# Performance work log

Measured on AMD Instinct MI355X. Metric: run time of the kernel, lower is better.

## Reference

```python
import jax, jax.numpy as jnp
import numpy as np

ENC, STR_H, CELL_H, ATTN = 512, 256, 512, 512
B, L = 64, 1024


def setup_inputs() -> dict:
    key = jax.random.key(0)
    ks = jax.random.split(key, 12)
    s = lambda fan_in: 1.0 / np.sqrt(fan_in)
    return {
        "encoded_features_map": jax.random.normal(ks[0], (B, L, ENC), jnp.float32),
        "structural_hidden_state": jax.random.normal(ks[1], (1, B, STR_H), jnp.float32),
        "cell_content_hidden_state": jax.random.normal(ks[2], (1, B, CELL_H), jnp.float32),
        "W_enc": jax.random.uniform(ks[3], (ENC, ATTN), jnp.float32, -s(ENC), s(ENC)),
        "b_enc": jax.random.uniform(ks[4], (ATTN,), jnp.float32, -s(ENC), s(ENC)),
        "W_str": jax.random.uniform(ks[5], (STR_H, ATTN), jnp.float32, -s(STR_H), s(STR_H)),
        "b_str": jax.random.uniform(ks[6], (ATTN,), jnp.float32, -s(STR_H), s(STR_H)),
        "W_cell": jax.random.uniform(ks[7], (CELL_H, ATTN), jnp.float32, -s(CELL_H), s(CELL_H)),
        "b_cell": jax.random.uniform(ks[8], (ATTN,), jnp.float32, -s(CELL_H), s(CELL_H)),
        "W_comb": jax.random.uniform(ks[9], (ATTN, 1), jnp.float32, -s(ATTN), s(ATTN)),
        "b_comb": jax.random.uniform(ks[10], (1,), jnp.float32, -s(ATTN), s(ATTN)),
    }


def reference(encoded_features_map, structural_hidden_state, cell_content_hidden_state,
              W_enc, b_enc, W_str, b_str, W_cell, b_cell, W_comb, b_comb):
    # [B, L, A] projection of encoder features
    a_enc = jnp.einsum("ble,ea->bla", encoded_features_map, W_enc) + b_enc
    # [B, A] projections of the two hidden states (squeeze layer dim)
    a_str = structural_hidden_state[0] @ W_str + b_str
    a_cell = cell_content_hidden_state[0] @ W_cell + b_cell
    # broadcast add + ReLU + scalar score: [B, L]
    h = jax.nn.relu(a_enc + a_str[:, None, :] + a_cell[:, None, :])
    scores = jnp.einsum("bla,ao->bl", h, W_comb) + b_comb[0]
    weights = jax.nn.softmax(scores, axis=1)  # over sequence dim
    # weighted sum over L -> [B, ENC]
    context = jnp.einsum("bl,ble->be", weights, encoded_features_map)
    return context
```

## Files before the change

### kernel.cpp

```cpp
#include <hip/hip_runtime.h>
#include <stdint.h>

#define ENC_D 512
#define ATTN_D 512
#define STR_D 256
#define CELL_D 512
#define BATCH 64
#define SEQ 1024
#define NROWS (BATCH * SEQ)

typedef __bf16 bf16x8 __attribute__((ext_vector_type(8)));
typedef float f32x4 __attribute__((ext_vector_type(4)));

__device__ __forceinline__ unsigned short f2bf(float f) {
    unsigned int u = __float_as_uint(f);
    u += 0x7fffu + ((u >> 16) & 1u);
    return (unsigned short)(u >> 16);
}

__device__ __forceinline__ void lds_cp16(void* l, const void* g) {
    __builtin_amdgcn_global_load_lds(
        (const __attribute__((address_space(1))) unsigned int*)g,
        (__attribute__((address_space(3))) unsigned int*)l, 16, 0, 0);
}

#define BAR_VM4() asm volatile("s_waitcnt vmcnt(4)\n\ts_barrier" ::: "memory")
#define BAR_VM0() asm volatile("s_waitcnt vmcnt(0)\n\ts_barrier" ::: "memory")

__global__ __launch_bounds__(256) void k_prep(const float* __restrict__ W,
                                              unsigned short* __restrict__ WF,
                                              const float* __restrict__ str,
                                              const float* __restrict__ cell,
                                              const float* __restrict__ Wstr,
                                              const float* __restrict__ Wcell,
                                              float* __restrict__ bpart,
                                              float* __restrict__ outz) {
    __shared__ char smraw[64 * 68 * 2];
    const int bx = blockIdx.x, t = threadIdx.x;

    if (bx < 64) {
        unsigned short* T = (unsigned short*)smraw;
        const int ei = bx >> 3, ni = bx & 7;
        const int e0 = ei * 64, n0 = ni * 64;
#pragma unroll
        for (int i = 0; i < 4; ++i) {
            const int idx = t + i * 256;
            const int r = idx >> 4, c4 = idx & 15;
            const float4 v = *(const float4*)(W + (size_t)(e0 + r) * ATTN_D + n0 + c4 * 4);
            T[(c4 * 4 + 0) * 68 + r] = f2bf(v.x);
            T[(c4 * 4 + 1) * 68 + r] = f2bf(v.y);
            T[(c4 * 4 + 2) * 68 + r] = f2bf(v.z);
            T[(c4 * 4 + 3) * 68 + r] = f2bf(v.w);
        }
        __syncthreads();
#pragma unroll
        for (int i = 0; i < 2; ++i) {
            const int q = t + i * 256;
            const int n = q >> 3, ge = q & 7;
            union { unsigned short s[8]; uint4 u; } o;
#pragma unroll
            for (int j = 0; j < 8; ++j) o.s[j] = T[n * 68 + ge * 8 + j];
            const int ng = n0 + n;
            const int g = ei * 8 + ge;
            const int nt = ng >> 4, c = ng & 15;
            const int ks = g >> 2, quad = g & 3;
            const int gi = nt * 1024 + ks * 64 + quad * 16 + c;
            *(uint4*)(WF + (size_t)gi * 8) = o.u;
        }
    } else if (bx < 832) {
        float* sj = (float*)smraw;
        float* red = (float*)smraw + 64;
        const int q = bx - 64;
        const int b = q / 12, jq = q - b * 12;
        const float* hvec;
        const float* Wbase;
        if (jq < 4) { hvec = str + b * STR_D + jq * 64;         Wbase = Wstr + (size_t)(jq * 64) * ATTN_D; }
        else        { hvec = cell + b * CELL_D + (jq - 4) * 64; Wbase = Wcell + (size_t)((jq - 4) * 64) * ATTN_D; }
        if (t < 64) sj[t] = hvec[t];
        __syncthreads();
        const int h = t >> 7, a4 = t & 127;
        f32x4 acc = {0.f, 0.f, 0.f, 0.f};
#pragma unroll 8
        for (int i = h * 32; i < h * 32 + 32; ++i) {
            const float s = sj[i];
            const float4 wv = *(const float4*)(Wbase + (size_t)i * ATTN_D + a4 * 4);
            acc[0] += s * wv.x; acc[1] += s * wv.y; acc[2] += s * wv.z; acc[3] += s * wv.w;
        }
        if (h == 1) *(f32x4*)(red + a4 * 4) = acc;
        __syncthreads();
        if (h == 0) {
            const f32x4 o = *(const f32x4*)(red + a4 * 4);
            acc[0] += o[0]; acc[1] += o[1]; acc[2] += o[2]; acc[3] += o[3];
            *(f32x4*)(bpart + (size_t)(jq * BATCH + b) * ATTN_D + a4 * 4) = acc;
        }
    } else {
        const f32x4 z = {0.f, 0.f, 0.f, 0.f};
        float* p = outz + (size_t)(bx - 832) * 2048 + t * 8;
        *(f32x4*)p = z;
        *(f32x4*)(p + 4) = z;
    }
}

__global__ __launch_bounds__(512, 1) void k_scores(const float* __restrict__ E,
                                                   const unsigned short* __restrict__ WF,
                                                   const float* __restrict__ bpart,
                                                   const float* __restrict__ b_enc,
                                                   const float* __restrict__ b_str,
                                                   const float* __restrict__ b_cell,
                                                   const float* __restrict__ Wcomb,
                                                   float* __restrict__ scores) {
    __shared__ unsigned short buf[3][16384];
    __shared__ float sbias[512];
    __shared__ float sWc[512];

    const int tid = threadIdx.x;
    const int r0 = blockIdx.x * 256;
    const int b = blockIdx.x >> 2;
    const int w = tid >> 6, lane = tid & 63;
    const int quad = lane >> 4, c = lane & 15;

#pragma unroll
    for (int p = 0; p < 2; ++p)
#pragma unroll
        for (int i = 0; i < 4; ++i)
            lds_cp16((char*)&buf[p][0] + i * 8192 + tid * 16,
                     (const char*)WF + (size_t)p * 32768 + i * 8192 + tid * 16);

    if (tid < 128) {
        const int a = tid * 4;
        const float4 be = *(const float4*)(b_enc + a);
        const float4 bs = *(const float4*)(b_str + a);
        const float4 bc = *(const float4*)(b_cell + a);
        f32x4 s;
        s[0] = be.x + bs.x + bc.x; s[1] = be.y + bs.y + bc.y;
        s[2] = be.z + bs.z + bc.z; s[3] = be.w + bs.w + bc.w;
#pragma unroll
        for (int jq = 0; jq < 12; ++jq) {
            const float4 p = *(const float4*)(bpart + (size_t)(jq * BATCH + b) * ATTN_D + a);
            s[0] += p.x; s[1] += p.y; s[2] += p.z; s[3] += p.w;
        }
        *(f32x4*)(sbias + a) = s;
        const float4 wcv = *(const float4*)(Wcomb + a);
        f32x4 wc4; wc4[0] = wcv.x; wc4[1] = wcv.y; wc4[2] = wcv.z; wc4[3] = wcv.w;
        *(f32x4*)(sWc + a) = wc4;
    }

    bf16x8 afr[2][16];
#pragma unroll
    for (int m = 0; m < 2; ++m) {
        const float* Ep = E + (size_t)(r0 + w * 32 + m * 16 + c) * ENC_D + quad * 8;
#pragma unroll
        for (int ks = 0; ks < 16; ++ks) {
            const float4 v0 = *(const float4*)(Ep + ks * 32);
            const float4 v1 = *(const float4*)(Ep + ks * 32 + 4);
            union { unsigned short s[8]; bf16x8 v; } u;
            u.s[0] = f2bf(v0.x); u.s[1] = f2bf(v0.y);
            u.s[2] = f2bf(v0.z); u.s[3] = f2bf(v0.w);
            u.s[4] = f2bf(v1.x); u.s[5] = f2bf(v1.y);
            u.s[6] = f2bf(v1.z); u.s[7] = f2bf(v1.w);
            afr[m][ks] = u.v;
        }
    }

    float sc0[4] = {0.f, 0.f, 0.f, 0.f};
    float sc1[4] = {0.f, 0.f, 0.f, 0.f};

    __syncthreads();

    int cbuf = 0, sbuf = 2;
    for (int ch = 0; ch < 16; ++ch) {
        if (ch < 14) {
            const char* gsrc = (const char*)WF + (size_t)(ch + 2) * 32768;
            char* ldst = (char*)&buf[sbuf][0];
#pragma unroll
            for (int i = 0; i < 4; ++i)
                lds_cp16(ldst + i * 8192 + tid * 16, gsrc + i * 8192 + tid * 16);
        }

        const unsigned short* wb = &buf[cbuf][0];
        f32x4 a0e = {0.f,0.f,0.f,0.f}, a0o = {0.f,0.f,0.f,0.f};
        f32x4 a1e = {0.f,0.f,0.f,0.f}, a1o = {0.f,0.f,0.f,0.f};
        f32x4 b0e = {0.f,0.f,0.f,0.f}, b0o = {0.f,0.f,0.f,0.f};
        f32x4 b1e = {0.f,0.f,0.f,0.f}, b1o = {0.f,0.f,0.f,0.f};
#pragma unroll
        for (int ks = 0; ks < 16; ks += 2) {
            const bf16x8 f0 = *(const bf16x8*)(wb + (ks * 64 + lane) * 8);
            const bf16x8 f1 = *(const bf16x8*)(wb + ((ks + 1) * 64 + lane) * 8);
            const bf16x8 g0 = *(const bf16x8*)(wb + 8192 + (ks * 64 + lane) * 8);
            const bf16x8 g1 = *(const bf16x8*)(wb + 8192 + ((ks + 1) * 64 + lane) * 8);
            a0e = __builtin_amdgcn_mfma_f32_16x16x32_bf16(afr[0][ks], f0, a0e, 0, 0, 0);
            a1e = __builtin_amdgcn_mfma_f32_16x16x32_bf16(afr[1][ks], f0, a1e, 0, 0, 0);
            a0o = __builtin_amdgcn_mfma_f32_16x16x32_bf16(afr[0][ks + 1], f1, a0o, 0, 0, 0);
            a1o = __builtin_amdgcn_mfma_f32_16x16x32_bf16(afr[1][ks + 1], f1, a1o, 0, 0, 0);
            b0e = __builtin_amdgcn_mfma_f32_16x16x32_bf16(afr[0][ks], g0, b0e, 0, 0, 0);
            b1e = __builtin_amdgcn_mfma_f32_16x16x32_bf16(afr[1][ks], g0, b1e, 0, 0, 0);
            b0o = __builtin_amdgcn_mfma_f32_16x16x32_bf16(afr[0][ks + 1], g1, b0o, 0, 0, 0);
            b1o = __builtin_amdgcn_mfma_f32_16x16x32_bf16(afr[1][ks + 1], g1, b1o, 0, 0, 0);
        }

        const int n0 = ch * 32 + c;
        const float bi0 = sbias[n0], wc0 = sWc[n0];
        const float bi1 = sbias[n0 + 16], wc1 = sWc[n0 + 16];
#pragma unroll
        for (int r = 0; r < 4; ++r) {
            float v;
            v = (a0e[r] + a0o[r]) + bi0; sc0[r] += (v > 0.f ? v : 0.f) * wc0;
            v = (b0e[r] + b0o[r]) + bi1; sc0[r] += (v > 0.f ? v : 0.f) * wc1;
            v = (a1e[r] + a1o[r]) + bi0; sc1[r] += (v > 0.f ? v : 0.f) * wc0;
            v = (b1e[r] + b1o[r]) + bi1; sc1[r] += (v > 0.f ? v : 0.f) * wc1;
        }

        cbuf = (cbuf == 2) ? 0 : cbuf + 1;
        sbuf = (sbuf == 2) ? 0 : sbuf + 1;
        if (ch < 15) {
            if (ch < 14) BAR_VM4();
            else         BAR_VM0();
        }
    }

#pragma unroll
    for (int r = 0; r < 4; ++r) {
        float v0 = sc0[r], v1 = sc1[r];
        v0 += __shfl_xor(v0, 1); v1 += __shfl_xor(v1, 1);
        v0 += __shfl_xor(v0, 2); v1 += __shfl_xor(v1, 2);
        v0 += __shfl_xor(v0, 4); v1 += __shfl_xor(v1, 4);
        sc0[r] = v0 + __shfl_xor(v0, 8);
        sc1[r] = v1 + __shfl_xor(v1, 8);
    }
    if (c == 0) {
        const int g0 = r0 + w * 32 + quad * 4;
#pragma unroll
        for (int r = 0; r < 4; ++r) scores[g0 + r] = sc0[r];
#pragma unroll
        for (int r = 0; r < 4; ++r) scores[g0 + 16 + r] = sc1[r];
    }
}

__global__ __launch_bounds__(128) void k_ctx(const float* __restrict__ E,
                                             const float* __restrict__ scores,
                                             float* __restrict__ out) {
    __shared__ float ex[1024];
    __shared__ float rtmp[4];
    const int blk = blockIdx.x, t = threadIdx.x;
    const int b = blk >> 4, lo = blk & 15;

    float v[8];
    float m = -1e30f;
#pragma unroll
    for (int i = 0; i < 8; ++i) {
        v[i] = scores[b * SEQ + i * 128 + t];
        m = fmaxf(m, v[i]);
    }
#pragma unroll
    for (int o = 32; o > 0; o >>= 1) m = fmaxf(m, __shfl_xor(m, o));
    if ((t & 63) == 0) rtmp[t >> 6] = m;
    __syncthreads();
    m = fmaxf(rtmp[0], rtmp[1]);

    float s = 0.f;
#pragma unroll
    for (int i = 0; i < 8; ++i) {
        const float e = __expf(v[i] - m);
        ex[i * 128 + t] = e;
        s += e;
    }
#pragma unroll
    for (int o = 32; o > 0; o >>= 1) s += __shfl_xor(s, o);
    if ((t & 63) == 0) rtmp[2 + (t >> 6)] = s;
    __syncthreads();
    const float inv = 1.f / (rtmp[2] + rtmp[3]);

    const float* Ep = E + (size_t)(b * SEQ + lo * 64) * ENC_D + t * 4;
    f32x4 acc = {0.f, 0.f, 0.f, 0.f};
#pragma unroll 8
    for (int l = 0; l < 64; ++l) {
        const float4 e4 = *(const float4*)(Ep + (size_t)l * ENC_D);
        const float wv = ex[lo * 64 + l];
        acc[0] += wv * e4.x; acc[1] += wv * e4.y;
        acc[2] += wv * e4.z; acc[3] += wv * e4.w;
    }
    float* op = out + b * ENC_D + t * 4;
    atomicAdd(op + 0, acc[0] * inv);
    atomicAdd(op + 1, acc[1] * inv);
    atomicAdd(op + 2, acc[2] * inv);
    atomicAdd(op + 3, acc[3] * inv);
}

extern "C" void kernel_launch(void* const* d_in, const int* in_sizes, int n_in,
                              void* d_out, int out_size, void* d_ws, size_t ws_size,
                              hipStream_t stream) {
    const float* E      = (const float*)d_in[0];
    const float* str    = (const float*)d_in[1];
    const float* cell   = (const float*)d_in[2];
    const float* Wenc   = (const float*)d_in[3];
    const float* b_enc  = (const float*)d_in[4];
    const float* Wstr   = (const float*)d_in[5];
    const float* b_str  = (const float*)d_in[6];
    const float* Wcell  = (const float*)d_in[7];
    const float* b_cell = (const float*)d_in[8];
    const float* Wcomb  = (const float*)d_in[9];
    float* out = (float*)d_out;

    char* ws = (char*)d_ws;
    unsigned short* WF = (unsigned short*)ws;
    float* scores = (float*)(ws + (512 << 10));
    float* bpart  = (float*)(ws + (512 << 10) + (256 << 10));

    k_prep<<<848, 256, 0, stream>>>(Wenc, WF, str, cell, Wstr, Wcell, bpart, out);
    k_scores<<<NROWS / 256, 512, 0, stream>>>(E, WF, bpart, b_enc, b_str, b_cell, Wcomb, scores);
    k_ctx<<<1024, 128, 0, stream>>>(E, scores, out);
}
```

Before: 275.1 us.

## Halve k_scores wavefronts with 64 rows per wave; split k_ctx over 256 threads

k_scores now runs 4 waves of 256 threads per block, each wave covering 64 rows (4 M-tiles) instead of 32, so every B-fragment read from LDS feeds 4 MFMAs. This cuts LDS read traffic per MFMA. The cost is that each thread holds twice as many A-fragment registers (64 bf16x8) and a block has fewer waves to hide latency. k_ctx moves to 256 threads, splitting the 64-row sequence chunk into two halves that are reduced through shared memory before the atomics, which adds memory-level parallelism.

```diff
diff --git a/kernel.cpp b/kernel.cpp
--- a/kernel.cpp
+++ b/kernel.cpp
@@ -24,7 +24,7 @@
         (__attribute__((address_space(3))) unsigned int*)l, 16, 0, 0);
 }
 
-#define BAR_VM4() asm volatile("s_waitcnt vmcnt(4)\n\ts_barrier" ::: "memory")
+#define BAR_VM8() asm volatile("s_waitcnt vmcnt(8)\n\ts_barrier" ::: "memory")
 #define BAR_VM0() asm volatile("s_waitcnt vmcnt(0)\n\ts_barrier" ::: "memory")
 
 __global__ __launch_bounds__(256) void k_prep(const float* __restrict__ W,
@@ -101,7 +101,7 @@
     }
 }
 
-__global__ __launch_bounds__(512, 1) void k_scores(const float* __restrict__ E,
+__global__ __launch_bounds__(256, 1) void k_scores(const float* __restrict__ E,
                                                    const unsigned short* __restrict__ WF,
                                                    const float* __restrict__ bpart,
                                                    const float* __restrict__ b_enc,
@@ -122,9 +122,9 @@
 #pragma unroll
     for (int p = 0; p < 2; ++p)
 #pragma unroll
-        for (int i = 0; i < 4; ++i)
-            lds_cp16((char*)&buf[p][0] + i * 8192 + tid * 16,
-                     (const char*)WF + (size_t)p * 32768 + i * 8192 + tid * 16);
+        for (int i = 0; i < 8; ++i)
+            lds_cp16((char*)&buf[p][0] + i * 4096 + tid * 16,
+                     (const char*)WF + (size_t)p * 32768 + i * 4096 + tid * 16);
 
     if (tid < 128) {
         const int a = tid * 4;
@@ -145,10 +145,10 @@
         *(f32x4*)(sWc + a) = wc4;
     }
 
-    bf16x8 afr[2][16];
-#pragma unroll
-    for (int m = 0; m < 2; ++m) {
-        const float* Ep = E + (size_t)(r0 + w * 32 + m * 16 + c) * ENC_D + quad * 8;
+    bf16x8 afr[4][16];
+#pragma unroll
+    for (int m = 0; m < 4; ++m) {
+        const float* Ep = E + (size_t)(r0 + w * 64 + m * 16 + c) * ENC_D + quad * 8;
 #pragma unroll
         for (int ks = 0; ks < 16; ++ks) {
             const float4 v0 = *(const float4*)(Ep + ks * 32);
@@ -162,8 +162,8 @@
         }
     }
 
-    float sc0[4] = {0.f, 0.f, 0.f, 0.f};
-    float sc1[4] = {0.f, 0.f, 0.f, 0.f};
+    float sc[4][4] = {{0.f, 0.f, 0.f, 0.f}, {0.f, 0.f, 0.f, 0.f},
+                      {0.f, 0.f, 0.f, 0.f}, {0.f, 0.f, 0.f, 0.f}};
 
     __syncthreads();
 
@@ -173,117 +173,123 @@
             const char* gsrc = (const char*)WF + (size_t)(ch + 2) * 32768;
             char* ldst = (char*)&buf[sbuf][0];
 #pragma unroll
-            for (int i = 0; i < 4; ++i)
-                lds_cp16(ldst + i * 8192 + tid * 16, gsrc + i * 8192 + tid * 16);
+            for (int i = 0; i < 8; ++i)
+                lds_cp16(ldst + i * 4096 + tid * 16, gsrc + i * 4096 + tid * 16);
         }
 
         const unsigned short* wb = &buf[cbuf][0];
-        f32x4 a0e = {0.f,0.f,0.f,0.f}, a0o = {0.f,0.f,0.f,0.f};
-        f32x4 a1e = {0.f,0.f,0.f,0.f}, a1o = {0.f,0.f,0.f,0.f};
-        f32x4 b0e = {0.f,0.f,0.f,0.f}, b0o = {0.f,0.f,0.f,0.f};
-        f32x4 b1e = {0.f,0.f,0.f,0.f}, b1o = {0.f,0.f,0.f,0.f};
-#pragma unroll
-        for (int ks = 0; ks < 16; ks += 2) {
+        const f32x4 z4 = {0.f, 0.f, 0.f, 0.f};
+        f32x4 acc0[4], acc1[4];
+#pragma unroll
+        for (int m = 0; m < 4; ++m) { acc0[m] = z4; acc1[m] = z4; }
+#pragma unroll
+        for (int ks = 0; ks < 16; ++ks) {
             const bf16x8 f0 = *(const bf16x8*)(wb + (ks * 64 + lane) * 8);
-            const bf16x8 f1 = *(const bf16x8*)(wb + ((ks + 1) * 64 + lane) * 8);
             const bf16x8 g0 = *(const bf16x8*)(wb + 8192 + (ks * 64 + lane) * 8);
-            const bf16x8 g1 = *(const bf16x8*)(wb + 8192 + ((ks + 1) * 64 + lane) * 8);
-            a0e = __builtin_amdgcn_mfma_f32_16x16x32_bf16(afr[0][ks], f0, a0e, 0, 0, 0);
-            a1e = __builtin_amdgcn_mfma_f32_16x16x32_bf16(afr[1][ks], f0, a1e, 0, 0, 0);
-            a0o = __builtin_amdgcn_mfma_f32_16x16x32_bf16(afr[0][ks + 1], f1, a0o, 0, 0, 0);
-            a1o = __builtin_amdgcn_mfma_f32_16x16x32_bf16(afr[1][ks + 1], f1, a1o, 0, 0, 0);
-            b0e = __builtin_amdgcn_mfma_f32_16x16x32_bf16(afr[0][ks], g0, b0e, 0, 0, 0);
-            b1e = __builtin_amdgcn_mfma_f32_16x16x32_bf16(afr[1][ks], g0, b1e, 0, 0, 0);
-            b0o = __builtin_amdgcn_mfma_f32_16x16x32_bf16(afr[0][ks + 1], g1, b0o, 0, 0, 0);
-            b1o = __builtin_amdgcn_mfma_f32_16x16x32_bf16(afr[1][ks + 1], g1, b1o, 0, 0, 0);
+#pragma unroll
+            for (int m = 0; m < 4; ++m) {
+                acc0[m] = __builtin_amdgcn_mfma_f32_16x16x32_bf16(afr[m][ks], f0, acc0[m], 0, 0, 0);
+                acc1[m] = __builtin_amdgcn_mfma_f32_16x16x32_bf16(afr[m][ks], g0, acc1[m], 0, 0, 0);
+            }
         }
 
         const int n0 = ch * 32 + c;
         const float bi0 = sbias[n0], wc0 = sWc[n0];
         const float bi1 = sbias[n0 + 16], wc1 = sWc[n0 + 16];
 #pragma unroll
-        for (int r = 0; r < 4; ++r) {
-            float v;
-            v = (a0e[r] + a0o[r]) + bi0; sc0[r] += (v > 0.f ? v : 0.f) * wc0;
-            v = (b0e[r] + b0o[r]) + bi1; sc0[r] += (v > 0.f ? v : 0.f) * wc1;
-            v = (a1e[r] + a1o[r]) + bi0; sc1[r] += (v > 0.f ? v : 0.f) * wc0;
-            v = (b1e[r] + b1o[r]) + bi1; sc1[r] += (v > 0.f ? v : 0.f) * wc1;
-        }
+        for (int m = 0; m < 4; ++m)
+#pragma unroll
+            for (int r = 0; r < 4; ++r) {
+                float v;
+                v = acc0[m][r] + bi0; sc[m][r] += (v > 0.f ? v : 0.f) * wc0;
+                v = acc1[m][r] + bi1; sc[m][r] += (v > 0.f ? v : 0.f) * wc1;
+            }
 
         cbuf = (cbuf == 2) ? 0 : cbuf + 1;
         sbuf = (sbuf == 2) ? 0 : sbuf + 1;
         if (ch < 15) {
-            if (ch < 14) BAR_VM4();
+            if (ch < 14) BAR_VM8();
             else         BAR_VM0();
         }
     }
 
 #pragma unroll
-    for (int r = 0; r < 4; ++r) {
-        float v0 = sc0[r], v1 = sc1[r];
-        v0 += __shfl_xor(v0, 1); v1 += __shfl_xor(v1, 1);
-        v0 += __shfl_xor(v0, 2); v1 += __shfl_xor(v1, 2);
-        v0 += __shfl_xor(v0, 4); v1 += __shfl_xor(v1, 4);
-        sc0[r] = v0 + __shfl_xor(v0, 8);
-        sc1[r] = v1 + __shfl_xor(v1, 8);
-    }
+    for (int m = 0; m < 4; ++m)
+#pragma unroll
+        for (int r = 0; r < 4; ++r) {
+            float v = sc[m][r];
+            v += __shfl_xor(v, 1);
+            v += __shfl_xor(v, 2);
+            v += __shfl_xor(v, 4);
+            v += __shfl_xor(v, 8);
+            sc[m][r] = v;
+        }
     if (c == 0) {
-        const int g0 = r0 + w * 32 + quad * 4;
-#pragma unroll
-        for (int r = 0; r < 4; ++r) scores[g0 + r] = sc0[r];
-#pragma unroll
-        for (int r = 0; r < 4; ++r) scores[g0 + 16 + r] = sc1[r];
-    }
-}
-
-__global__ __launch_bounds__(128) void k_ctx(const float* __restrict__ E,
+        const int g0 = r0 + w * 64 + quad * 4;
+#pragma unroll
+        for (int m = 0; m < 4; ++m)
+#pragma unroll
+            for (int r = 0; r < 4; ++r)
+                scores[g0 + m * 16 + r] = sc[m][r];
+    }
+}
+
+__global__ __launch_bounds__(256) void k_ctx(const float* __restrict__ E,
                                              const float* __restrict__ scores,
                                              float* __restrict__ out) {
     __shared__ float ex[1024];
-    __shared__ float rtmp[4];
+    __shared__ float red[512];
+    __shared__ float rtmp[8];
     const int blk = blockIdx.x, t = threadIdx.x;
     const int b = blk >> 4, lo = blk & 15;
-
-    float v[8];
+    const int wv = t >> 6;
+
+    float v[4];
     float m = -1e30f;
 #pragma unroll
-    for (int i = 0; i < 8; ++i) {
-        v[i] = scores[b * SEQ + i * 128 + t];
+    for (int i = 0; i < 4; ++i) {
+        v[i] = scores[b * SEQ + i * 256 + t];
         m = fmaxf(m, v[i]);
     }
 #pragma unroll
     for (int o = 32; o > 0; o >>= 1) m = fmaxf(m, __shfl_xor(m, o));
-    if ((t & 63) == 0) rtmp[t >> 6] = m;
+    if ((t & 63) == 0) rtmp[wv] = m;
     __syncthreads();
-    m = fmaxf(rtmp[0], rtmp[1]);
+    m = fmaxf(fmaxf(rtmp[0], rtmp[1]), fmaxf(rtmp[2], rtmp[3]));
 
     float s = 0.f;
 #pragma unroll
-    for (int i = 0; i < 8; ++i) {
+    for (int i = 0; i < 4; ++i) {
         const float e = __expf(v[i] - m);
-        ex[i * 128 + t] = e;
+        ex[i * 256 + t] = e;
         s += e;
     }
 #pragma unroll
     for (int o = 32; o > 0; o >>= 1) s += __shfl_xor(s, o);
-    if ((t & 63) == 0) rtmp[2 + (t >> 6)] = s;
+    if ((t & 63) == 0) rtmp[4 + wv] = s;
     __syncthreads();
-    const float inv = 1.f / (rtmp[2] + rtmp[3]);
-
-    const float* Ep = E + (size_t)(b * SEQ + lo * 64) * ENC_D + t * 4;
+    const float inv = 1.f / (rtmp[4] + rtmp[5] + rtmp[6] + rtmp[7]);
+
+    const int h = t >> 7, c = t & 127;
+    const float* Ep = E + (size_t)(b * SEQ + lo * 64 + h * 32) * ENC_D + c * 4;
     f32x4 acc = {0.f, 0.f, 0.f, 0.f};
 #pragma unroll 8
-    for (int l = 0; l < 64; ++l) {
+    for (int l = 0; l < 32; ++l) {
         const float4 e4 = *(const float4*)(Ep + (size_t)l * ENC_D);
-        const float wv = ex[lo * 64 + l];
-        acc[0] += wv * e4.x; acc[1] += wv * e4.y;
-        acc[2] += wv * e4.z; acc[3] += wv * e4.w;
-    }
-    float* op = out + b * ENC_D + t * 4;
-    atomicAdd(op + 0, acc[0] * inv);
-    atomicAdd(op + 1, acc[1] * inv);
-    atomicAdd(op + 2, acc[2] * inv);
-    atomicAdd(op + 3, acc[3] * inv);
+        const float wgt = ex[lo * 64 + h * 32 + l];
+        acc[0] += wgt * e4.x; acc[1] += wgt * e4.y;
+        acc[2] += wgt * e4.z; acc[3] += wgt * e4.w;
+    }
+    if (h == 1) *(f32x4*)(red + c * 4) = acc;
+    __syncthreads();
+    if (h == 0) {
+        const f32x4 o4 = *(const f32x4*)(red + c * 4);
+        float* op = out + b * ENC_D + c * 4;
+        atomicAdd(op + 0, (acc[0] + o4[0]) * inv);
+        atomicAdd(op + 1, (acc[1] + o4[1]) * inv);
+        atomicAdd(op + 2, (acc[2] + o4[2]) * inv);
+        atomicAdd(op + 3, (acc[3] + o4[3]) * inv);
+    }
 }
 
 extern "C" void kernel_launch(void* const* d_in, const int* in_sizes, int n_in,
@@ -307,6 +313,6 @@
     float* bpart  = (float*)(ws + (512 << 10) + (256 << 10));
 
     k_prep<<<848, 256, 0, stream>>>(Wenc, WF, str, cell, Wstr, Wcell, bpart, out);
-    k_scores<<<NROWS / 256, 512, 0, stream>>>(E, WF, bpart, b_enc, b_str, b_cell, Wcomb, scores);
-    k_ctx<<<1024, 128, 0, stream>>>(E, scores, out);
-}
+    k_scores<<<NROWS / 256, 256, 0, stream>>>(E, WF, bpart, b_enc, b_str, b_cell, Wcomb, scores);
+    k_ctx<<<1024, 256, 0, stream>>>(E, scores, out);
+}
```

Result: slower. 280.8 us (+2.1%).

## Fuse softmax and context reduction into scores kernel with split-softmax merge

Applied to the files above, without the earlier changes.

Each scores block now computes a local softmax over its 256 rows and immediately accumulates the weighted context sum from the same E rows, writing partial context and (max, sum) stats. A small final kernel rescales and merges the four partials per batch, replacing the separate context kernel, atomics, and output zeroing. This aims to avoid a second full pass over the encoder features from DRAM while the rows are likely still cached, at the cost of extra work and barriers at the tail of the scores kernel.

```diff
diff --git a/kernel.cpp b/kernel.cpp
--- a/kernel.cpp
+++ b/kernel.cpp
@@ -33,8 +33,7 @@
                                               const float* __restrict__ cell,
                                               const float* __restrict__ Wstr,
                                               const float* __restrict__ Wcell,
-                                              float* __restrict__ bpart,
-                                              float* __restrict__ outz) {
+                                              float* __restrict__ bpart) {
     __shared__ char smraw[64 * 68 * 2];
     const int bx = blockIdx.x, t = threadIdx.x;
 
@@ -67,7 +66,7 @@
             const int gi = nt * 1024 + ks * 64 + quad * 16 + c;
             *(uint4*)(WF + (size_t)gi * 8) = o.u;
         }
-    } else if (bx < 832) {
+    } else {
         float* sj = (float*)smraw;
         float* red = (float*)smraw + 64;
         const int q = bx - 64;
@@ -93,11 +92,6 @@
             acc[0] += o[0]; acc[1] += o[1]; acc[2] += o[2]; acc[3] += o[3];
             *(f32x4*)(bpart + (size_t)(jq * BATCH + b) * ATTN_D + a4 * 4) = acc;
         }
-    } else {
-        const f32x4 z = {0.f, 0.f, 0.f, 0.f};
-        float* p = outz + (size_t)(bx - 832) * 2048 + t * 8;
-        *(f32x4*)p = z;
-        *(f32x4*)(p + 4) = z;
     }
 }
 
@@ -108,10 +102,15 @@
                                                    const float* __restrict__ b_str,
                                                    const float* __restrict__ b_cell,
                                                    const float* __restrict__ Wcomb,
-                                                   float* __restrict__ scores) {
+                                                   float* __restrict__ ctxp,
+                                                   float* __restrict__ stats) {
     __shared__ unsigned short buf[3][16384];
     __shared__ float sbias[512];
     __shared__ float sWc[512];
+    __shared__ float sx[256];
+    __shared__ float ex[256];
+    __shared__ float red[3][512];
+    __shared__ float rtmp[8];
 
     const int tid = threadIdx.x;
     const int r0 = blockIdx.x * 256;
@@ -228,62 +227,86 @@
         sc1[r] = v1 + __shfl_xor(v1, 8);
     }
     if (c == 0) {
-        const int g0 = r0 + w * 32 + quad * 4;
-#pragma unroll
-        for (int r = 0; r < 4; ++r) scores[g0 + r] = sc0[r];
-#pragma unroll
-        for (int r = 0; r < 4; ++r) scores[g0 + 16 + r] = sc1[r];
-    }
-}
-
-__global__ __launch_bounds__(128) void k_ctx(const float* __restrict__ E,
-                                             const float* __restrict__ scores,
-                                             float* __restrict__ out) {
-    __shared__ float ex[1024];
-    __shared__ float rtmp[4];
-    const int blk = blockIdx.x, t = threadIdx.x;
-    const int b = blk >> 4, lo = blk & 15;
-
-    float v[8];
-    float m = -1e30f;
-#pragma unroll
-    for (int i = 0; i < 8; ++i) {
-        v[i] = scores[b * SEQ + i * 128 + t];
-        m = fmaxf(m, v[i]);
-    }
-#pragma unroll
-    for (int o = 32; o > 0; o >>= 1) m = fmaxf(m, __shfl_xor(m, o));
-    if ((t & 63) == 0) rtmp[t >> 6] = m;
+        const int l0 = w * 32 + quad * 4;
+#pragma unroll
+        for (int r = 0; r < 4; ++r) sx[l0 + r] = sc0[r];
+#pragma unroll
+        for (int r = 0; r < 4; ++r) sx[l0 + 16 + r] = sc1[r];
+    }
     __syncthreads();
-    m = fmaxf(rtmp[0], rtmp[1]);
-
-    float s = 0.f;
-#pragma unroll
-    for (int i = 0; i < 8; ++i) {
-        const float e = __expf(v[i] - m);
-        ex[i * 128 + t] = e;
-        s += e;
-    }
-#pragma unroll
-    for (int o = 32; o > 0; o >>= 1) s += __shfl_xor(s, o);
-    if ((t & 63) == 0) rtmp[2 + (t >> 6)] = s;
+
+    if (tid < 256) {
+        float v = sx[tid];
+        float mm = v;
+#pragma unroll
+        for (int o = 32; o > 0; o >>= 1) mm = fmaxf(mm, __shfl_xor(mm, o));
+        if (lane == 0) rtmp[w] = mm;
+    }
     __syncthreads();
-    const float inv = 1.f / (rtmp[2] + rtmp[3]);
-
-    const float* Ep = E + (size_t)(b * SEQ + lo * 64) * ENC_D + t * 4;
-    f32x4 acc = {0.f, 0.f, 0.f, 0.f};
+    const float m_p = fmaxf(fmaxf(rtmp[0], rtmp[1]), fmaxf(rtmp[2], rtmp[3]));
+    if (tid < 256) {
+        const float e = __expf(sx[tid] - m_p);
+        ex[tid] = e;
+        float ss = e;
+#pragma unroll
+        for (int o = 32; o > 0; o >>= 1) ss += __shfl_xor(ss, o);
+        if (lane == 0) rtmp[4 + w] = ss;
+    }
+    __syncthreads();
+    if (tid == 0) {
+        stats[blockIdx.x * 2 + 0] = m_p;
+        stats[blockIdx.x * 2 + 1] = rtmp[4] + rtmp[5] + rtmp[6] + rtmp[7];
+    }
+
+    {
+        const int g = tid >> 7, col4 = tid & 127;
+        const float* Ep = E + (size_t)(r0 + g * 64) * ENC_D + col4 * 4;
+        f32x4 acc = {0.f, 0.f, 0.f, 0.f};
 #pragma unroll 8
-    for (int l = 0; l < 64; ++l) {
-        const float4 e4 = *(const float4*)(Ep + (size_t)l * ENC_D);
-        const float wv = ex[lo * 64 + l];
-        acc[0] += wv * e4.x; acc[1] += wv * e4.y;
-        acc[2] += wv * e4.z; acc[3] += wv * e4.w;
-    }
-    float* op = out + b * ENC_D + t * 4;
-    atomicAdd(op + 0, acc[0] * inv);
-    atomicAdd(op + 1, acc[1] * inv);
-    atomicAdd(op + 2, acc[2] * inv);
-    atomicAdd(op + 3, acc[3] * inv);
+        for (int l = 0; l < 64; ++l) {
+            const float4 e4 = *(const float4*)(Ep + (size_t)l * ENC_D);
+            const float wgt = ex[g * 64 + l];
+            acc[0] += wgt * e4.x; acc[1] += wgt * e4.y;
+            acc[2] += wgt * e4.z; acc[3] += wgt * e4.w;
+        }
+        if (g > 0) *(f32x4*)(&red[g - 1][col4 * 4]) = acc;
+        __syncthreads();
+        if (g == 0) {
+            const f32x4 r1 = *(const f32x4*)(&red[0][col4 * 4]);
+            const f32x4 r2 = *(const f32x4*)(&red[1][col4 * 4]);
+            const f32x4 r3 = *(const f32x4*)(&red[2][col4 * 4]);
+            acc[0] += r1[0] + r2[0] + r3[0];
+            acc[1] += r1[1] + r2[1] + r3[1];
+            acc[2] += r1[2] + r2[2] + r3[2];
+            acc[3] += r1[3] + r2[3] + r3[3];
+            *(f32x4*)(ctxp + (size_t)blockIdx.x * 512 + col4 * 4) = acc;
+        }
+    }
+}
+
+__global__ __launch_bounds__(128) void k_final(const float* __restrict__ ctxp,
+                                               const float* __restrict__ stats,
+                                               float* __restrict__ out) {
+    const int b = blockIdx.x, t = threadIdx.x;
+    const float m0 = stats[(b * 4 + 0) * 2], z0 = stats[(b * 4 + 0) * 2 + 1];
+    const float m1 = stats[(b * 4 + 1) * 2], z1 = stats[(b * 4 + 1) * 2 + 1];
+    const float m2 = stats[(b * 4 + 2) * 2], z2 = stats[(b * 4 + 2) * 2 + 1];
+    const float m3 = stats[(b * 4 + 3) * 2], z3 = stats[(b * 4 + 3) * 2 + 1];
+    const float m = fmaxf(fmaxf(m0, m1), fmaxf(m2, m3));
+    const float a0 = __expf(m0 - m), a1 = __expf(m1 - m);
+    const float a2 = __expf(m2 - m), a3 = __expf(m3 - m);
+    const float invD = 1.f / (z0 * a0 + z1 * a1 + z2 * a2 + z3 * a3);
+
+    const float4 c0 = *(const float4*)(ctxp + (size_t)(b * 4 + 0) * 512 + t * 4);
+    const float4 c1 = *(const float4*)(ctxp + (size_t)(b * 4 + 1) * 512 + t * 4);
+    const float4 c2 = *(const float4*)(ctxp + (size_t)(b * 4 + 2) * 512 + t * 4);
+    const float4 c3 = *(const float4*)(ctxp + (size_t)(b * 4 + 3) * 512 + t * 4);
+    f32x4 o;
+    o[0] = (c0.x * a0 + c1.x * a1 + c2.x * a2 + c3.x * a3) * invD;
+    o[1] = (c0.y * a0 + c1.y * a1 + c2.y * a2 + c3.y * a3) * invD;
+    o[2] = (c0.z * a0 + c1.z * a1 + c2.z * a2 + c3.z * a3) * invD;
+    o[3] = (c0.w * a0 + c1.w * a1 + c2.w * a2 + c3.w * a3) * invD;
+    *(f32x4*)(out + (size_t)b * ENC_D + t * 4) = o;
 }
 
 extern "C" void kernel_launch(void* const* d_in, const int* in_sizes, int n_in,
@@ -303,10 +326,11 @@
 
     char* ws = (char*)d_ws;
     unsigned short* WF = (unsigned short*)ws;
-    float* scores = (float*)(ws + (512 << 10));
-    float* bpart  = (float*)(ws + (512 << 10) + (256 << 10));
-
-    k_prep<<<848, 256, 0, stream>>>(Wenc, WF, str, cell, Wstr, Wcell, bpart, out);
-    k_scores<<<NROWS / 256, 512, 0, stream>>>(E, WF, bpart, b_enc, b_str, b_cell, Wcomb, scores);
-    k_ctx<<<1024, 128, 0, stream>>>(E, scores, out);
-}
+    float* bpart = (float*)(ws + (512 << 10));
+    float* ctxp  = (float*)(ws + (512 << 10) + (1536 << 10));
+    float* stats = (float*)(ws + (512 << 10) + (2048 << 10));
+
+    k_prep<<<832, 256, 0, stream>>>(Wenc, WF, str, cell, Wstr, Wcell, bpart);
+    k_scores<<<NROWS / 256, 512, 0, stream>>>(E, WF, bpart, b_enc, b_str, b_cell, Wcomb, ctxp, stats);
+    k_final<<<BATCH, 128, 0, stream>>>(ctxp, stats, out);
+}
```

Result: no change. 270.0 us (-1.9%).
